# Performance work log

Hardware: AMD Instinct MI355X
Metric: run time of the kernel (lower is better)

The kernel has to match this reference:

```python
import jax, jax.numpy as jnp
import numpy as np

BS, C, H, W = 8, 128, 64, 64
CH = C // 2  # proj output channels


def setup_inputs() -> dict:
    key = jax.random.key(0)
    ks = jax.random.split(key, 8)
    s = 1.0 / np.sqrt(C)
    return {
        "tgt": jax.random.normal(ks[0], (BS, C, H, W), dtype=jnp.float32),
        "ref": jax.random.normal(ks[1], (BS, C, H, W), dtype=jnp.float32),
        "W_tgt": jax.random.normal(ks[2], (CH, C), dtype=jnp.float32) * s,
        "b_tgt": jax.random.normal(ks[3], (CH,), dtype=jnp.float32) * s,
        "W_ref": jax.random.normal(ks[4], (CH, C), dtype=jnp.float32) * s,
        "b_ref": jax.random.normal(ks[5], (CH,), dtype=jnp.float32) * s,
        "W_out": jax.random.normal(ks[6], (C, C), dtype=jnp.float32) * s,
        "b_out": jax.random.normal(ks[7], (C,), dtype=jnp.float32) * s,
    }


def reference(tgt, ref, W_tgt, b_tgt, W_ref, b_ref, W_out, b_out):
    bs, c, h, w = tgt.shape
    n = h * w
    # 1x1 conv == per-pixel matmul over channels; flatten spatial to tokens
    tgt_f = tgt.reshape(bs, c, n)              # [bs, c, n]
    ref_f = ref.reshape(bs, c, n)              # [bs, c, n]
    # att_tgt: [bs, n, c/2] ; att_ref: [bs, c/2, n] (ReLU after proj)
    att_tgt = jax.nn.relu(jnp.einsum('bcn,oc->bno', tgt_f, W_tgt) + b_tgt)
    att_ref = jax.nn.relu(jnp.einsum('bcn,oc->bon', ref_f, W_ref) + b_ref[None, :, None])
    pre_att = jnp.einsum('bnd,bdm->bnm', att_tgt, att_ref)   # [bs, n, n]
    att = jax.nn.softmax(pre_att, axis=-1)
    # fused tokens: [bs, n, c] = att @ ref_tokens
    fused = jnp.einsum('bnm,bcm->bnc', att, ref_f)
    fused = fused.transpose(0, 2, 1).reshape(bs, c, h, w)
    # output gate: 1x1 conv on tgt (no activation), elementwise mul
    att_out = jnp.einsum('bcn,oc->bon', tgt_f, W_out) + b_out[None, :, None]
    fused = fused * att_out.reshape(bs, c, h, w)
    return fused
```

## Files before the change

### kernel.cpp

```cpp
#include <hip/hip_runtime.h>

typedef __attribute__((ext_vector_type(8))) _Float16 f16x8;
typedef __attribute__((ext_vector_type(4))) float f32x4;
typedef __attribute__((ext_vector_type(16))) float f32x16;

constexpr int kC  = 128;
constexpr int kCH = 64;
constexpr int kN  = 4096;
constexpr float kLog2e = 1.4426950408889634f;

__device__ __forceinline__ unsigned pkrtz(float a, float b) {
    union { __fp16 __attribute__((ext_vector_type(2))) v; unsigned u; } cv;
    cv.v = __builtin_amdgcn_cvt_pkrtz(a, b);
    return cv.u;
}

__device__ __forceinline__ float x2(float x) {
    return __builtin_amdgcn_exp2f(x);
}

__device__ __forceinline__ float hadd2(unsigned u) {
    union { unsigned v; _Float16 h[2]; } c; c.v = u;
    return (float)c.h[0] + (float)c.h[1];
}

__device__ __forceinline__ void g2l16(const unsigned short* g, unsigned short* l) {
    __builtin_amdgcn_global_load_lds(
        (const __attribute__((address_space(1))) unsigned int*)(g),
        (__attribute__((address_space(3))) unsigned int*)(l),
        16, 0, 0);
}

__global__ __launch_bounds__(256, 2) void proj_fused(
    const float* __restrict__ tgt, const float* __restrict__ ref,
    const float* __restrict__ Wt, const float* __restrict__ Wr,
    const float* __restrict__ Wo, const float* __restrict__ bt,
    const float* __restrict__ br, const float* __restrict__ bo,
    unsigned short* __restrict__ Qw, unsigned short* __restrict__ Kw,
    unsigned short* __restrict__ Vw, float* __restrict__ Gw)
{
    __shared__ __align__(16) unsigned short Xs[2][64 * 128];
    const int t = threadIdx.x;
    const int sl2 = blockIdx.y >> 3;
    const int b = blockIdx.y & 7;
    const int tok0 = blockIdx.x << 7;

    const int w = t >> 6, lane = t & 63;
    const int lg = (lane >> 4) & 3, lm = lane & 15;

    const float* X = sl2 ? ref : tgt;
    const float* Xb0 = X + ((size_t)b * kC) * kN + tok0;
    unsigned short* Vout = Vw + ((size_t)b * kC) * kN + tok0;

    const float* Wqk  = sl2 ? Wr : Wt;
    const float* bqk  = sl2 ? br : bt;
    const float scale = sl2 ? 1.0f : kLog2e;

    f16x8 wfq[4];
    float bq[4];
    {
        const int ocb = w * 16;
        #pragma unroll
        for (int ks = 0; ks < 4; ++ks) {
            const float* wp = Wqk + (size_t)(ocb + lm) * kC + ks * 32 + lg * 8;
            f32x4 f0 = *(const f32x4*)wp;
            f32x4 f1 = *(const f32x4*)(wp + 4);
            union { f16x8 h; uint4 u; } cv;
            cv.u = make_uint4(pkrtz(f0[0] * scale, f0[1] * scale),
                              pkrtz(f0[2] * scale, f0[3] * scale),
                              pkrtz(f1[0] * scale, f1[1] * scale),
                              pkrtz(f1[2] * scale, f1[3] * scale));
            wfq[ks] = cv.h;
        }
        #pragma unroll
        for (int r = 0; r < 4; ++r) bq[r] = bqk[ocb + lg * 4 + r] * scale;
    }

    f16x8 wfg[2][4];
    float bg[2][4];
    if (sl2 == 0) {
        const int ocb = w * 32;
        #pragma unroll
        for (int ot = 0; ot < 2; ++ot) {
            const int oc = ocb + ot * 16 + lm;
            #pragma unroll
            for (int ks = 0; ks < 4; ++ks) {
                const float* wp = Wo + (size_t)oc * kC + ks * 32 + lg * 8;
                f32x4 f0 = *(const f32x4*)wp;
                f32x4 f1 = *(const f32x4*)(wp + 4);
                union { f16x8 h; uint4 u; } cv;
                cv.u = make_uint4(pkrtz(f0[0], f0[1]), pkrtz(f0[2], f0[3]),
                                  pkrtz(f1[0], f1[1]), pkrtz(f1[2], f1[3]));
                wfg[ot][ks] = cv.h;
            }
            #pragma unroll
            for (int r = 0; r < 4; ++r) bg[ot][r] = bo[ocb + ot * 16 + lg * 4 + r];
        }
    }

    const int tk4 = (t & 15) * 4;
    const int c8  = (t >> 4) * 8;

    auto loadX = [&](int toff, f32x4* xv) {
        #pragma unroll
        for (int j = 0; j < 8; ++j)
            xv[j] = *(const f32x4*)(Xb0 + (size_t)(c8 + j) * kN + toff + tk4);
    };
    auto stageX = [&](const f32x4* xv, unsigned short* Xsb, int toff) {
        if (sl2 == 1) {
            #pragma unroll
            for (int j = 0; j < 8; ++j)
                *(uint2*)(Vout + (size_t)(c8 + j) * kN + toff + tk4) =
                    make_uint2(pkrtz(xv[j][0], xv[j][1]), pkrtz(xv[j][2], xv[j][3]));
        }
        #pragma unroll
        for (int s = 0; s < 4; ++s) {
            const int tok = tk4 + s;
            const int cc = (c8 >> 3) ^ (tok & 7);
            uint4 pk;
            pk.x = pkrtz(xv[0][s], xv[1][s]);
            pk.y = pkrtz(xv[2][s], xv[3][s]);
            pk.z = pkrtz(xv[4][s], xv[5][s]);
            pk.w = pkrtz(xv[6][s], xv[7][s]);
            *(uint4*)(Xsb + tok * 128 + cc * 8) = pk;
        }
    };
    auto compute = [&](const unsigned short* Xsb, int tokb) {
        unsigned short* outp = (sl2 ? Kw : Qw) + ((size_t)b * kN + tokb) * kCH;
        float* Gb = Gw + ((size_t)b * kC) * kN + tokb;
        const int ocq = w * 16;
        const int ocg = w * 32;
        #pragma unroll
        for (int ns = 0; ns < 4; ++ns) {
            const int tok = ns * 16 + lm;
            f16x8 xf[4];
            #pragma unroll
            for (int ks = 0; ks < 4; ++ks)
                xf[ks] = *(const f16x8*)(Xsb + tok * 128 +
                                         (((ks * 4 + lg) ^ (tok & 7)) << 3));
            {
                f32x4 acc = {bq[0], bq[1], bq[2], bq[3]};
                #pragma unroll
                for (int ks = 0; ks < 4; ++ks)
                    acc = __builtin_amdgcn_mfma_f32_16x16x32_f16(wfq[ks], xf[ks], acc, 0, 0, 0);
                uint2 pk;
                pk.x = pkrtz(fmaxf(acc[0], 0.f), fmaxf(acc[1], 0.f));
                pk.y = pkrtz(fmaxf(acc[2], 0.f), fmaxf(acc[3], 0.f));
                *(uint2*)(outp + (size_t)tok * kCH + ocq + lg * 4) = pk;
            }
            if (sl2 == 0) {
                #pragma unroll
                for (int ot = 0; ot < 2; ++ot) {
                    f32x4 acc = {bg[ot][0], bg[ot][1], bg[ot][2], bg[ot][3]};
                    #pragma unroll
                    for (int ks = 0; ks < 4; ++ks)
                        acc = __builtin_amdgcn_mfma_f32_16x16x32_f16(wfg[ot][ks], xf[ks], acc, 0, 0, 0);
                    #pragma unroll
                    for (int r = 0; r < 4; ++r)
                        Gb[(size_t)(ocg + ot * 16 + lg * 4 + r) * kN + tok] = acc[r];
                }
            }
        }
    };

    f32x4 xv[8], xw[8];
    loadX(0, xv);
    stageX(xv, Xs[0], 0);
    __syncthreads();
    loadX(64, xw);
    compute(Xs[0], tok0);
    stageX(xw, Xs[1], 64);
    __syncthreads();
    compute(Xs[1], tok0 + 64);
}

__global__ __launch_bounds__(256, 2) void flash11_kernel(
    const unsigned short* __restrict__ Qw,
    const unsigned short* __restrict__ Kw,
    const unsigned short* __restrict__ Vw,
    const float* __restrict__ Gw,
    float* __restrict__ out)
{
    __shared__ __align__(16) unsigned short Ks[2][64 * 64];
    __shared__ __align__(16) unsigned short Vs[2][128 * 64];
    __shared__ float2 mlb[4][32];

    const int t = threadIdx.x;
    const int b  = blockIdx.x & 7;
    const int n0 = (blockIdx.x >> 3) << 6;
    const int w = t >> 6, lane = t & 63;
    const int qg = w >> 1, kh = w & 1;
    const int lq = lane & 31, hh = lane >> 5;
    const int n0q = n0 + qg * 32 + lq;

    const unsigned short* Qb = Qw + ((size_t)b * kN + n0q) * kCH;
    const unsigned short* Kb = Kw + ((size_t)b * kN) * kCH;
    const unsigned short* Vb = Vw + ((size_t)b * kC) * kN;

    f16x8 qf[4];
    #pragma unroll
    for (int st = 0; st < 4; ++st)
        qf[st] = *(const f16x8*)(Qb + st * 16 + hh * 8);

    const int srow = t >> 3, scol = t & 7;
    const int sco  = (scol ^ (srow & 7)) << 3;
    const int wv   = t >> 6;

    int ka[4];
    #pragma unroll
    for (int st = 0; st < 4; ++st)
        ka[st] = (kh * 32 + lq) * 64 + (((2 * st + hh) ^ (lq & 7)) << 3);
    int va[4][2];
    #pragma unroll
    for (int cb = 0; cb < 4; ++cb)
        #pragma unroll
        for (int s = 0; s < 2; ++s)
            va[cb][s] = (cb * 32 + lq) * 64 + (((kh * 4 + 2 * s + hh) ^ (lq & 7)) << 3);

    f32x16 O[4];
    #pragma unroll
    for (int cb = 0; cb < 4; ++cb)
        #pragma unroll
        for (int r = 0; r < 16; ++r) O[cb][r] = 0.f;
    float L = 0.f, m_run = 0.f;

    unsigned short* Ks0 = Ks[0]; unsigned short* Ks1 = Ks[1];
    unsigned short* Vs0 = Vs[0]; unsigned short* Vs1 = Vs[1];

    auto stage = [&](unsigned short* Kd, unsigned short* Vd, int m0) {
        g2l16(Kb + (size_t)(m0 + srow) * kCH + sco,      Kd + wv * 512);
        g2l16(Kb + (size_t)(m0 + 32 + srow) * kCH + sco, Kd + 2048 + wv * 512);
        #pragma unroll
        for (int j = 0; j < 4; ++j)
            g2l16(Vb + (size_t)(32 * j + srow) * kN + m0 + sco,
                  Vd + j * 2048 + wv * 512);
    };
    stage(Ks0, Vs0, 0);

    auto tile = [&](const unsigned short* Kc, const unsigned short* Vc,
                    unsigned short* Kn, unsigned short* Vn, int kt) {
        __syncthreads();
        if (kt + 1 < kN / 64) stage(Kn, Vn, (kt + 1) << 6);

        f32x16 sa;
        #pragma unroll
        for (int r = 0; r < 16; ++r) sa[r] = 0.f;
        __builtin_amdgcn_s_setprio(1);
        #pragma unroll
        for (int st = 0; st < 4; ++st) {
            f16x8 kf = *(const f16x8*)(Kc + ka[st]);
            sa = __builtin_amdgcn_mfma_f32_32x32x16_f16(kf, qf[st], sa, 0, 0, 0);
        }
        __builtin_amdgcn_s_setprio(0);

        float mh = sa[0];
        #pragma unroll
        for (int r = 1; r < 16; ++r) mh = fmaxf(mh, sa[r]);
        const float mq = fmaxf(mh, __shfl_xor(mh, 32));
        const bool resc = __any(mq > m_run + 8.0f);
        const float mnew = resc ? fmaxf(m_run, mq) : m_run;

        #pragma unroll
        for (int r = 0; r < 16; ++r) sa[r] = x2(sa[r] - mnew);
        unsigned P[8];
        #pragma unroll
        for (int i = 0; i < 8; ++i) P[i] = pkrtz(sa[2 * i], sa[2 * i + 1]);

        float ps = 0.f;
        #pragma unroll
        for (int i = 0; i < 8; ++i) ps += hadd2(P[i]);
        ps += __shfl_xor(ps, 32);

        if (resc) {
            const float al = x2(m_run - mnew);
            #pragma unroll
            for (int cb = 0; cb < 4; ++cb) O[cb] *= al;
            L = L * al + ps;
            m_run = mnew;
        } else {
            L += ps;
        }

        f16x8 pf[2];
        #pragma unroll
        for (int s = 0; s < 2; ++s) {
            unsigned xa = __shfl_xor(P[4 * s + 0], 32);
            unsigned xb = __shfl_xor(P[4 * s + 1], 32);
            unsigned xc = __shfl_xor(P[4 * s + 2], 32);
            unsigned xd = __shfl_xor(P[4 * s + 3], 32);
            uint4 fu;
            fu.x = hh ? xc : P[4 * s + 0];
            fu.y = hh ? xd : P[4 * s + 1];
            fu.z = hh ? P[4 * s + 2] : xa;
            fu.w = hh ? P[4 * s + 3] : xb;
            union { uint4 u; f16x8 h; } cv; cv.u = fu;
            pf[s] = cv.h;
        }

        __builtin_amdgcn_s_setprio(1);
        #pragma unroll
        for (int cb = 0; cb < 4; ++cb) {
            #pragma unroll
            for (int s = 0; s < 2; ++s) {
                f16x8 vf = *(const f16x8*)(Vc + va[cb][s]);
                O[cb] = __builtin_amdgcn_mfma_f32_32x32x16_f16(vf, pf[s], O[cb], 0, 0, 0);
            }
        }
        __builtin_amdgcn_s_setprio(0);
    };

    for (int kt = 0; kt < kN / 64; kt += 2) {
        tile(Ks0, Vs0, Ks1, Vs1, kt);
        tile(Ks1, Vs1, Ks0, Vs0, kt + 1);
    }

    __syncthreads();
    mlb[w][lq] = make_float2(m_run, L);
    __syncthreads();
    const float2 pml = mlb[w ^ 1][lq];
    const float mt = fmaxf(m_run, pml.x);
    const float a  = x2(m_run - mt);
    const float Lt = L * a + pml.y * x2(pml.x - mt);

    float* Obuf = (float*)Vs;
    const int obase = qg * 4096 + lane * 64;
    #pragma unroll
    for (int cb = 0; cb < 4; ++cb) O[cb] *= a;

    if (kh) {
        #pragma unroll
        for (int c = 0; c < 16; ++c) {
            const int cb = c >> 2, q4 = c & 3;
            *(float4*)(Obuf + obase + (((c + lane) & 15) << 2)) =
                make_float4(O[cb][q4 * 4 + 0], O[cb][q4 * 4 + 1],
                            O[cb][q4 * 4 + 2], O[cb][q4 * 4 + 3]);
        }
    }
    __syncthreads();
    if (!kh) {
        #pragma unroll
        for (int c = 0; c < 16; ++c) {
            const int cb = c >> 2, q4 = c & 3;
            float4 p = *(const float4*)(Obuf + obase + (((c + lane) & 15) << 2));
            O[cb][q4 * 4 + 0] += p.x;
            O[cb][q4 * 4 + 1] += p.y;
            O[cb][q4 * 4 + 2] += p.z;
            O[cb][q4 * 4 + 3] += p.w;
        }
        const float inv = 1.0f / Lt;
        const float* Gb = Gw + ((size_t)b * kC + 4 * hh) * kN + n0 + qg * 32 + lq;
        float*       Ob = out + ((size_t)b * kC + 4 * hh) * kN + n0 + qg * 32 + lq;
        #pragma unroll
        for (int cb = 0; cb < 4; ++cb) {
            #pragma unroll
            for (int r = 0; r < 16; ++r) {
                const int coff = cb * 32 + (r & 3) + 8 * (r >> 2);
                Ob[(size_t)coff * kN] = O[cb][r] * inv * Gb[(size_t)coff * kN];
            }
        }
    }
}

extern "C" void kernel_launch(void* const* d_in, const int* in_sizes, int n_in,
                              void* d_out, int out_size, void* d_ws, size_t ws_size,
                              hipStream_t stream) {
    const float* tgt   = (const float*)d_in[0];
    const float* ref   = (const float*)d_in[1];
    const float* W_tgt = (const float*)d_in[2];
    const float* b_tgt = (const float*)d_in[3];
    const float* W_ref = (const float*)d_in[4];
    const float* b_ref = (const float*)d_in[5];
    const float* W_out = (const float*)d_in[6];
    const float* b_out = (const float*)d_in[7];
    float* out = (float*)d_out;

    const size_t QK = (size_t)8 * kN * kCH;
    const size_t CV = (size_t)8 * kC * kN;
    unsigned short* Qw = (unsigned short*)d_ws;
    unsigned short* Kw = Qw + QK;
    unsigned short* Vw = Kw + QK;
    float*          Gw = (float*)(Vw + CV);

    proj_fused<<<dim3(32, 16), 256, 0, stream>>>(tgt, ref, W_tgt, W_ref, W_out,
                                                 b_tgt, b_ref, b_out, Qw, Kw, Vw, Gw);
    flash11_kernel<<<dim3(512), 256, 0, stream>>>(Qw, Kw, Vw, Gw, out);
}
```

Measured before the change: 182.1 us.

## Software-pipeline the PV matmul one tile behind softmax; use permlane32 swaps

```diff
diff --git a/kernel.cpp b/kernel.cpp
--- a/kernel.cpp
+++ b/kernel.cpp
@@ -3,6 +3,7 @@
 typedef __attribute__((ext_vector_type(8))) _Float16 f16x8;
 typedef __attribute__((ext_vector_type(4))) float f32x4;
 typedef __attribute__((ext_vector_type(16))) float f32x16;
+typedef __attribute__((ext_vector_type(2))) unsigned u32x2;
 
 constexpr int kC  = 128;
 constexpr int kCH = 64;
@@ -22,6 +23,19 @@
 __device__ __forceinline__ float hadd2(unsigned u) {
     union { unsigned v; _Float16 h[2]; } c; c.v = u;
     return (float)c.h[0] + (float)c.h[1];
+}
+
+__device__ __forceinline__ u32x2 pl32(unsigned a, unsigned b) {
+    return __builtin_amdgcn_permlane32_swap(a, b, false, false);
+}
+__device__ __forceinline__ u32x2 pl32x(float v) {
+    float c;
+    asm("v_mov_b32 %0, %1" : "=&v"(c) : "v"(v));
+    union { float f; unsigned u; } a, b2; a.f = v; b2.f = c;
+    return pl32(a.u, b2.u);
+}
+__device__ __forceinline__ float uf(unsigned u) {
+    union { unsigned v; float f; } c; c.v = u; return c.f;
 }
 
 __device__ __forceinline__ void g2l16(const unsigned short* g, unsigned short* l) {
@@ -174,7 +188,7 @@
     compute(Xs[1], tok0 + 64);
 }
 
-__global__ __launch_bounds__(256, 2) void flash11_kernel(
+__global__ __launch_bounds__(256, 2) void flash12_kernel(
     const unsigned short* __restrict__ Qw,
     const unsigned short* __restrict__ Kw,
     const unsigned short* __restrict__ Vw,
@@ -182,7 +196,7 @@
     float* __restrict__ out)
 {
     __shared__ __align__(16) unsigned short Ks[2][64 * 64];
-    __shared__ __align__(16) unsigned short Vs[2][128 * 64];
+    __shared__ __align__(16) unsigned short Vs[3][128 * 64];
     __shared__ float2 mlb[4][32];
 
     const int t = threadIdx.x;
@@ -224,8 +238,12 @@
         for (int r = 0; r < 16; ++r) O[cb][r] = 0.f;
     float L = 0.f, m_run = 0.f;
 
-    unsigned short* Ks0 = Ks[0]; unsigned short* Ks1 = Ks[1];
-    unsigned short* Vs0 = Vs[0]; unsigned short* Vs1 = Vs[1];
+    f16x8 pfp[2];
+    {
+        union { uint4 u; f16x8 h; } z;
+        z.u = make_uint4(0u, 0u, 0u, 0u);
+        pfp[0] = z.h; pfp[1] = z.h;
+    }
 
     auto stage = [&](unsigned short* Kd, unsigned short* Vd, int m0) {
         g2l16(Kb + (size_t)(m0 + srow) * kCH + sco,      Kd + wv * 512);
@@ -235,10 +253,12 @@
             g2l16(Vb + (size_t)(32 * j + srow) * kN + m0 + sco,
                   Vd + j * 2048 + wv * 512);
     };
-    stage(Ks0, Vs0, 0);
-
-    auto tile = [&](const unsigned short* Kc, const unsigned short* Vc,
-                    unsigned short* Kn, unsigned short* Vn, int kt) {
+
+    unsigned short *Kt = Ks[0], *Kn = Ks[1];
+    unsigned short *Vp = Vs[2], *Vt = Vs[0], *Vn = Vs[1];
+    stage(Kt, Vt, 0);
+
+    for (int kt = 0; kt < kN / 64; ++kt) {
         __syncthreads();
         if (kt + 1 < kN / 64) stage(Kn, Vn, (kt + 1) << 6);
 
@@ -248,7 +268,7 @@
         __builtin_amdgcn_s_setprio(1);
         #pragma unroll
         for (int st = 0; st < 4; ++st) {
-            f16x8 kf = *(const f16x8*)(Kc + ka[st]);
+            f16x8 kf = *(const f16x8*)(Kt + ka[st]);
             sa = __builtin_amdgcn_mfma_f32_32x32x16_f16(kf, qf[st], sa, 0, 0, 0);
         }
         __builtin_amdgcn_s_setprio(0);
@@ -256,20 +276,34 @@
         float mh = sa[0];
         #pragma unroll
         for (int r = 1; r < 16; ++r) mh = fmaxf(mh, sa[r]);
-        const float mq = fmaxf(mh, __shfl_xor(mh, 32));
+        u32x2 mr = pl32x(mh);
+        const float mq = fmaxf(uf(mr[0]), uf(mr[1]));
         const bool resc = __any(mq > m_run + 8.0f);
         const float mnew = resc ? fmaxf(m_run, mq) : m_run;
 
+        __builtin_amdgcn_s_setprio(1);
+        if (kt > 0) {
+            #pragma unroll
+            for (int cb = 0; cb < 4; ++cb) {
+                #pragma unroll
+                for (int s = 0; s < 2; ++s) {
+                    f16x8 vf = *(const f16x8*)(Vp + va[cb][s]);
+                    O[cb] = __builtin_amdgcn_mfma_f32_32x32x16_f16(vf, pfp[s], O[cb], 0, 0, 0);
+                }
+            }
+        }
+        __builtin_amdgcn_s_setprio(0);
+
         #pragma unroll
         for (int r = 0; r < 16; ++r) sa[r] = x2(sa[r] - mnew);
         unsigned P[8];
         #pragma unroll
         for (int i = 0; i < 8; ++i) P[i] = pkrtz(sa[2 * i], sa[2 * i + 1]);
-
         float ps = 0.f;
         #pragma unroll
         for (int i = 0; i < 8; ++i) ps += hadd2(P[i]);
-        ps += __shfl_xor(ps, 32);
+        u32x2 pr = pl32x(ps);
+        ps = uf(pr[0]) + uf(pr[1]);
 
         if (resc) {
             const float al = x2(m_run - mnew);
@@ -281,38 +315,29 @@
             L += ps;
         }
 
-        f16x8 pf[2];
         #pragma unroll
         for (int s = 0; s < 2; ++s) {
-            unsigned xa = __shfl_xor(P[4 * s + 0], 32);
-            unsigned xb = __shfl_xor(P[4 * s + 1], 32);
-            unsigned xc = __shfl_xor(P[4 * s + 2], 32);
-            unsigned xd = __shfl_xor(P[4 * s + 3], 32);
-            uint4 fu;
-            fu.x = hh ? xc : P[4 * s + 0];
-            fu.y = hh ? xd : P[4 * s + 1];
-            fu.z = hh ? P[4 * s + 2] : xa;
-            fu.w = hh ? P[4 * s + 3] : xb;
-            union { uint4 u; f16x8 h; } cv; cv.u = fu;
-            pf[s] = cv.h;
-        }
-
-        __builtin_amdgcn_s_setprio(1);
-        #pragma unroll
-        for (int cb = 0; cb < 4; ++cb) {
-            #pragma unroll
-            for (int s = 0; s < 2; ++s) {
-                f16x8 vf = *(const f16x8*)(Vc + va[cb][s]);
-                O[cb] = __builtin_amdgcn_mfma_f32_32x32x16_f16(vf, pf[s], O[cb], 0, 0, 0);
-            }
-        }
-        __builtin_amdgcn_s_setprio(0);
-    };
-
-    for (int kt = 0; kt < kN / 64; kt += 2) {
-        tile(Ks0, Vs0, Ks1, Vs1, kt);
-        tile(Ks1, Vs1, Ks0, Vs0, kt + 1);
-    }
+            u32x2 r0 = pl32(P[4 * s + 0], P[4 * s + 2]);
+            u32x2 r1 = pl32(P[4 * s + 1], P[4 * s + 3]);
+            union { uint4 u; f16x8 h; } cv;
+            cv.u = make_uint4(r0[0], r1[0], r0[1], r1[1]);
+            pfp[s] = cv.h;
+        }
+
+        unsigned short* tv = Vp; Vp = Vt; Vt = Vn; Vn = tv;
+        unsigned short* tk = Kt; Kt = Kn; Kn = tk;
+    }
+
+    __builtin_amdgcn_s_setprio(1);
+    #pragma unroll
+    for (int cb = 0; cb < 4; ++cb) {
+        #pragma unroll
+        for (int s = 0; s < 2; ++s) {
+            f16x8 vf = *(const f16x8*)(Vp + va[cb][s]);
+            O[cb] = __builtin_amdgcn_mfma_f32_32x32x16_f16(vf, pfp[s], O[cb], 0, 0, 0);
+        }
+    }
+    __builtin_amdgcn_s_setprio(0);
 
     __syncthreads();
     mlb[w][lq] = make_float2(m_run, L);
@@ -383,5 +408,5 @@
 
     proj_fused<<<dim3(32, 16), 256, 0, stream>>>(tgt, ref, W_tgt, W_ref, W_out,
                                                  b_tgt, b_ref, b_out, Qw, Kw, Vw, Gw);
-    flash11_kernel<<<dim3(512), 256, 0, stream>>>(Qw, Kw, Vw, Gw, out);
-}
+    flash12_kernel<<<dim3(512), 256, 0, stream>>>(Qw, Kw, Vw, Gw, out);
+}
```

Result: faster. 174.6 us (-4.1%).
